# Optimization experiments

Measured on AMD Instinct MI355X. Metric: run time of the kernel, lower is better.

Reference implementation:

```python
import jax, jax.numpy as jnp
import numpy as np

BATCH, SEQ_LEN, NUM_TAGS = 1024, 512, 48


def setup_inputs() -> dict:
    key = jax.random.key(0)
    k1, k2 = jax.random.split(key)
    potentials = jax.random.normal(k1, (BATCH, SEQ_LEN, NUM_TAGS), dtype=jnp.float32)
    transition_params = jax.random.normal(k2, (NUM_TAGS, NUM_TAGS), dtype=jnp.float32)
    return {"potentials": potentials, "transition_params": transition_params}


def reference(potentials, transition_params):
    """Viterbi forward decode for a linear-chain CRF.

    potentials: [B, T, num_tags] unary potentials.
    transition_params: [num_tags, num_tags] binary potentials.
    Returns:
      backpointers: [B, T-1, num_tags] int32 argmax backpointers.
      scores: [B, num_tags] final Viterbi scores.
    """
    init_state = potentials[:, 0]                 # [B, num_tags]
    rest = jnp.swapaxes(potentials[:, 1:], 0, 1)  # [T-1, B, num_tags]

    def step(state, inputs):
        # state: [B, num_tags]; inputs: [B, num_tags]
        # transition_scores[b, i, j] = state[b, i] + trans[i, j]
        transition_scores = state[:, :, None] + transition_params[None]  # [B, tags, tags]
        new_state = inputs + jnp.max(transition_scores, axis=1)          # [B, tags]
        backpointers = jnp.argmax(transition_scores, axis=1).astype(jnp.int32)
        return new_state, backpointers

    final_state, backpointers = jax.lax.scan(step, init_state, rest)
    backpointers = jnp.swapaxes(backpointers, 0, 1)  # [B, T-1, num_tags]
    return backpointers, final_state
```

## Files before the change

kernel.cpp:

```cpp
#include <hip/hip_runtime.h>


constexpr int B_ = 1024;
constexpr int T_ = 512;
constexpr int K_ = 48;
constexpr int C_ = 6;

__device__ __forceinline__ int min3i(int a, int b, int c) {
    int m = a < b ? a : b;
    return m < c ? m : c;
}

__global__ __launch_bounds__(64, 1) void crf_viterbi_kernel(
    const float* __restrict__ pot,
    const float* __restrict__ trans,
    float* __restrict__ out)
{
    const int b = blockIdx.x;
    const int j = threadIdx.x;

    __shared__ __align__(16) float stv[K_];

    float tcol[K_];
    #pragma unroll
    for (int i = 0; i < K_; ++i) tcol[i] = trans[i * K_ + j];

    const float* pp = pot + (size_t)b * T_ * K_ + j;
    float* bpp      = out + (size_t)b * (T_ - 1) * K_ + j;
    float* scout    = out + (size_t)B_ * (T_ - 1) * K_ + (size_t)b * K_ + j;

    float myst = pp[0];
    stv[j] = myst;
    __builtin_amdgcn_wave_barrier();

    float bpf0 = 0.0f, bpf1 = 0.0f, bpf2 = 0.0f,
          bpf3 = 0.0f, bpf4 = 0.0f, bpf5 = 0.0f;

#define STEP(PCUR, BPV)                                                        \
    do {                                                                       \
         \
        float4 sv[12];                                                         \
        const float4* stv4 = (const float4*)stv;                               \
        _Pragma("unroll")                                                      \
        for (int c = 0; c < 12; ++c) sv[c] = stv4[c];                          \
                      \
        float cand[K_];                                                        \
        _Pragma("unroll")                                                      \
        for (int c = 0; c < 12; ++c) {                                         \
            cand[4 * c + 0] = sv[c].x + tcol[4 * c + 0];                       \
            cand[4 * c + 1] = sv[c].y + tcol[4 * c + 1];                       \
            cand[4 * c + 2] = sv[c].z + tcol[4 * c + 2];                       \
            cand[4 * c + 3] = sv[c].w + tcol[4 * c + 3];                       \
        }                                                                      \
         \
        float m1[16];                                                          \
        _Pragma("unroll")                                                      \
        for (int k = 0; k < 16; ++k)                                           \
            m1[k] = fmaxf(fmaxf(cand[3 * k], cand[3 * k + 1]), cand[3 * k + 2]); \
        float m2[6];                                                           \
        _Pragma("unroll")                                                      \
        for (int k = 0; k < 5; ++k)                                            \
            m2[k] = fmaxf(fmaxf(m1[3 * k], m1[3 * k + 1]), m1[3 * k + 2]);     \
        m2[5] = m1[15];                                                        \
        float mm = fmaxf(fmaxf(fmaxf(m2[0], m2[1]), m2[2]),                    \
                         fmaxf(fmaxf(m2[3], m2[4]), m2[5]));                   \
           \
        myst = (PCUR) + mm;                                                    \
        stv[j] = myst;                                                         \
        __builtin_amdgcn_wave_barrier();                                       \
            \
        int e[K_];                                                             \
        _Pragma("unroll")                                                      \
        for (int i = 0; i < K_; ++i) e[i] = (cand[i] == mm) ? i : 63;          \
        int n1[16];                                                            \
        _Pragma("unroll")                                                      \
        for (int k = 0; k < 16; ++k)                                           \
            n1[k] = min3i(e[3 * k], e[3 * k + 1], e[3 * k + 2]);               \
        int n2[6];                                                             \
        _Pragma("unroll")                                                      \
        for (int k = 0; k < 5; ++k)                                            \
            n2[k] = min3i(n1[3 * k], n1[3 * k + 1], n1[3 * k + 2]);            \
        n2[5] = n1[15];                                                        \
        int n30 = min3i(n2[0], n2[1], n2[2]);                                  \
        int n31 = min3i(n2[3], n2[4], n2[5]);                                  \
        int xx = n30 < n31 ? n30 : n31;                                        \
        BPV = (float)xx;                                                       \
        *bpp = BPV;                                            \
        bpp += K_;                                                             \
    } while (0)

    float p1 = pp[(size_t)1 * K_];
    float pbuf[C_];
    #pragma unroll
    for (int u = 0; u < C_; ++u) pbuf[u] = pp[(size_t)(2 + u) * K_];

    STEP(p1, bpf5);

    for (int t0 = 2; t0 < T_; t0 += C_) {
        float pc[C_];
        #pragma unroll
        for (int u = 0; u < C_; ++u) pc[u] = pbuf[u];

        #pragma unroll
        for (int u = 0; u < C_; ++u) {
            int tn = t0 + C_ + u;
            if (tn > T_ - 1) tn = T_ - 1;
            pbuf[u] = pp[(size_t)tn * K_];
        }

        STEP(pc[0], bpf0);
        STEP(pc[1], bpf1);
        STEP(pc[2], bpf2);
        STEP(pc[3], bpf3);
        STEP(pc[4], bpf4);
        STEP(pc[5], bpf5);
    }

    asm volatile("" :: "v"(bpf0), "v"(bpf1), "v"(bpf2),
                       "v"(bpf3), "v"(bpf4), "v"(bpf5));

    *scout = myst;
#undef STEP
}

extern "C" void kernel_launch(void* const* d_in, const int* in_sizes, int n_in,
                              void* d_out, int out_size, void* d_ws, size_t ws_size,
                              hipStream_t stream) {
    const float* pot   = (const float*)d_in[0];
    const float* trans = (const float*)d_in[1];
    float* out         = (float*)d_out;
    crf_viterbi_kernel<<<dim3(B_), dim3(K_), 0, stream>>>(pot, trans, out);
}
```

Baseline: 322.7 us.

## Broadcast Viterbi state via readlane instead of LDS round-trip

Replaces the shared-memory state exchange (LDS write, wave barrier, 12 float4 LDS reads) with 48 v_readlane broadcasts of each lane's state into scalar registers. This takes the LDS latency and barrier off the serial per-timestep dependency chain. The change also hoists the backpointer store offsets to constant per-step offsets, replaces the clamped prefetch with a guarded pointer-increment load, and adds a waves_per_eu hint. The cost is 48 readlane instructions per step, which may need SGPR-to-VGPR handling and can add issue pressure.

```diff
diff --git a/kernel.cpp b/kernel.cpp
--- a/kernel.cpp
+++ b/kernel.cpp
@@ -11,15 +11,15 @@
     return m < c ? m : c;
 }
 
-__global__ __launch_bounds__(64, 1) void crf_viterbi_kernel(
+__global__ __launch_bounds__(64, 1)
+__attribute__((amdgpu_waves_per_eu(1, 1)))
+void crf_viterbi_kernel(
     const float* __restrict__ pot,
     const float* __restrict__ trans,
     float* __restrict__ out)
 {
     const int b = blockIdx.x;
     const int j = threadIdx.x;
-
-    __shared__ __align__(16) float stv[K_];
 
     float tcol[K_];
     #pragma unroll
@@ -30,29 +30,23 @@
     float* scout    = out + (size_t)B_ * (T_ - 1) * K_ + (size_t)b * K_ + j;
 
     float myst = pp[0];
-    stv[j] = myst;
-    __builtin_amdgcn_wave_barrier();
 
     float bpf0 = 0.0f, bpf1 = 0.0f, bpf2 = 0.0f,
           bpf3 = 0.0f, bpf4 = 0.0f, bpf5 = 0.0f;
 
-#define STEP(PCUR, BPV)                                                        \
+#define STEP(PCUR, UOFF, BPV)                                                  \
     do {                                                                       \
-         \
-        float4 sv[12];                                                         \
-        const float4* stv4 = (const float4*)stv;                               \
+                \
+        float s[K_];                                                           \
         _Pragma("unroll")                                                      \
-        for (int c = 0; c < 12; ++c) sv[c] = stv4[c];                          \
-                      \
+        for (int i = 0; i < K_; ++i)                                           \
+            s[i] = __int_as_float(                                             \
+                __builtin_amdgcn_readlane(__float_as_int(myst), i));           \
+                                    \
         float cand[K_];                                                        \
         _Pragma("unroll")                                                      \
-        for (int c = 0; c < 12; ++c) {                                         \
-            cand[4 * c + 0] = sv[c].x + tcol[4 * c + 0];                       \
-            cand[4 * c + 1] = sv[c].y + tcol[4 * c + 1];                       \
-            cand[4 * c + 2] = sv[c].z + tcol[4 * c + 2];                       \
-            cand[4 * c + 3] = sv[c].w + tcol[4 * c + 3];                       \
-        }                                                                      \
-         \
+        for (int i = 0; i < K_; ++i) cand[i] = s[i] + tcol[i];                 \
+              \
         float m1[16];                                                          \
         _Pragma("unroll")                                                      \
         for (int k = 0; k < 16; ++k)                                           \
@@ -64,11 +58,7 @@
         m2[5] = m1[15];                                                        \
         float mm = fmaxf(fmaxf(fmaxf(m2[0], m2[1]), m2[2]),                    \
                          fmaxf(fmaxf(m2[3], m2[4]), m2[5]));                   \
-           \
-        myst = (PCUR) + mm;                                                    \
-        stv[j] = myst;                                                         \
-        __builtin_amdgcn_wave_barrier();                                       \
-            \
+                      \
         int e[K_];                                                             \
         _Pragma("unroll")                                                      \
         for (int i = 0; i < K_; ++i) e[i] = (cand[i] == mm) ? i : 63;          \
@@ -85,35 +75,38 @@
         int n31 = min3i(n2[3], n2[4], n2[5]);                                  \
         int xx = n30 < n31 ? n30 : n31;                                        \
         BPV = (float)xx;                                                       \
-        *bpp = BPV;                                            \
-        bpp += K_;                                                             \
+        bpp[(UOFF) * K_] = BPV;        \
+                \
+        myst = (PCUR) + mm;                                                    \
     } while (0)
 
     float p1 = pp[(size_t)1 * K_];
     float pbuf[C_];
     #pragma unroll
     for (int u = 0; u < C_; ++u) pbuf[u] = pp[(size_t)(2 + u) * K_];
+    const float* pld = pp + (size_t)8 * K_;
 
-    STEP(p1, bpf5);
+    STEP(p1, 0, bpf5);
+    bpp += K_;
 
     for (int t0 = 2; t0 < T_; t0 += C_) {
         float pc[C_];
         #pragma unroll
         for (int u = 0; u < C_; ++u) pc[u] = pbuf[u];
 
-        #pragma unroll
-        for (int u = 0; u < C_; ++u) {
-            int tn = t0 + C_ + u;
-            if (tn > T_ - 1) tn = T_ - 1;
-            pbuf[u] = pp[(size_t)tn * K_];
+        if (t0 < T_ - C_) {
+            #pragma unroll
+            for (int u = 0; u < C_; ++u) pbuf[u] = pld[(size_t)u * K_];
+            pld += (size_t)C_ * K_;
         }
 
-        STEP(pc[0], bpf0);
-        STEP(pc[1], bpf1);
-        STEP(pc[2], bpf2);
-        STEP(pc[3], bpf3);
-        STEP(pc[4], bpf4);
-        STEP(pc[5], bpf5);
+        STEP(pc[0], 0, bpf0);
+        STEP(pc[1], 1, bpf1);
+        STEP(pc[2], 2, bpf2);
+        STEP(pc[3], 3, bpf3);
+        STEP(pc[4], 4, bpf4);
+        STEP(pc[5], 5, bpf5);
+        bpp += (size_t)C_ * K_;
     }
 
     asm volatile("" :: "v"(bpf0), "v"(bpf1), "v"(bpf2),
```

New measurement: 354.9 us. +10.0%, slower.

## Defer argmax backpointer scan by one step to overlap with next max chain

Applied to the files above, without the earlier changes.

The argmax backpointer scan for step t now runs during step t+1, after the shared-state load and off the critical max chain, using double-buffered candidate arrays. The argmax reduction becomes four independent descending select chains instead of compare-then-min trees. Transition columns are stored as float2 pairs, and the potential prefetch uses a running pointer with a guard instead of clamped indices. The aim is to shorten the serial latency per time step, at the cost of more live registers for two candidate buffers.

```diff
diff --git a/kernel.cpp b/kernel.cpp
--- a/kernel.cpp
+++ b/kernel.cpp
@@ -11,6 +11,8 @@
     return m < c ? m : c;
 }
 
+#define C2(A, i) ((i) & 1 ? A[(i) >> 1].y : A[(i) >> 1].x)
+
 __global__ __launch_bounds__(64, 1) void crf_viterbi_kernel(
     const float* __restrict__ pot,
     const float* __restrict__ trans,
@@ -21,42 +23,68 @@
 
     __shared__ __align__(16) float stv[K_];
 
-    float tcol[K_];
+    float2 tcol2[K_ / 2];
     #pragma unroll
-    for (int i = 0; i < K_; ++i) tcol[i] = trans[i * K_ + j];
+    for (int i = 0; i < K_ / 2; ++i)
+        tcol2[i] = make_float2(trans[(2 * i) * K_ + j],
+                               trans[(2 * i + 1) * K_ + j]);
 
     const float* pp = pot + (size_t)b * T_ * K_ + j;
-    float* bpp      = out + (size_t)b * (T_ - 1) * K_ + j;
+    float* bpc      = out + (size_t)b * (T_ - 1) * K_ + j;
     float* scout    = out + (size_t)B_ * (T_ - 1) * K_ + (size_t)b * K_ + j;
 
     float myst = pp[0];
     stv[j] = myst;
     __builtin_amdgcn_wave_barrier();
 
+    float2 candA2[K_ / 2], candB2[K_ / 2];
+    float mmA = 0.0f, mmB = 0.0f;
+
     float bpf0 = 0.0f, bpf1 = 0.0f, bpf2 = 0.0f,
           bpf3 = 0.0f, bpf4 = 0.0f, bpf5 = 0.0f;
 
-#define STEP(PCUR, BPV)                                                        \
+#define SCAN4(CO2, MMO, XXDST)                                                 \
+    do {                                                                       \
+        int xx0 = 63, xx1 = 63, xx2 = 63, xx3 = 63;                            \
+        _Pragma("unroll")                                                      \
+        for (int i = 11; i >= 0; --i)  xx0 = (C2(CO2, i) == (MMO)) ? i : xx0;  \
+        _Pragma("unroll")                                                      \
+        for (int i = 23; i >= 12; --i) xx1 = (C2(CO2, i) == (MMO)) ? i : xx1;  \
+        _Pragma("unroll")                                                      \
+        for (int i = 35; i >= 24; --i) xx2 = (C2(CO2, i) == (MMO)) ? i : xx2;  \
+        _Pragma("unroll")                                                      \
+        for (int i = 47; i >= 36; --i) xx3 = (C2(CO2, i) == (MMO)) ? i : xx3;  \
+        XXDST = min3i(xx0, xx1, xx2) < xx3 ? min3i(xx0, xx1, xx2) : xx3;       \
+    } while (0)
+
+#define STEP(PCUR, CN2, CO2, MMN, MMO, DOSH, UOFF, BPV)                        \
     do {                                                                       \
          \
         float4 sv[12];                                                         \
         const float4* stv4 = (const float4*)stv;                               \
         _Pragma("unroll")                                                      \
         for (int c = 0; c < 12; ++c) sv[c] = stv4[c];                          \
-                      \
-        float cand[K_];                                                        \
+         \
+        if (DOSH) {                                                            \
+            int xx;                                                            \
+            SCAN4(CO2, MMO, xx);                                               \
+            BPV = (float)xx;                                                   \
+            bpc[(UOFF) * K_] = BPV;                \
+        }                                                                      \
+                   \
         _Pragma("unroll")                                                      \
         for (int c = 0; c < 12; ++c) {                                         \
-            cand[4 * c + 0] = sv[c].x + tcol[4 * c + 0];                       \
-            cand[4 * c + 1] = sv[c].y + tcol[4 * c + 1];                       \
-            cand[4 * c + 2] = sv[c].z + tcol[4 * c + 2];                       \
-            cand[4 * c + 3] = sv[c].w + tcol[4 * c + 3];                       \
+            CN2[2 * c]     = make_float2(sv[c].x + tcol2[2 * c].x,             \
+                                         sv[c].y + tcol2[2 * c].y);            \
+            CN2[2 * c + 1] = make_float2(sv[c].z + tcol2[2 * c + 1].x,         \
+                                         sv[c].w + tcol2[2 * c + 1].y);        \
         }                                                                      \
          \
         float m1[16];                                                          \
         _Pragma("unroll")                                                      \
         for (int k = 0; k < 16; ++k)                                           \
-            m1[k] = fmaxf(fmaxf(cand[3 * k], cand[3 * k + 1]), cand[3 * k + 2]); \
+            m1[k] = fmaxf(fmaxf(C2(CN2, 3 * k), C2(CN2, 3 * k + 1)),           \
+                          C2(CN2, 3 * k + 2));                                 \
         float m2[6];                                                           \
         _Pragma("unroll")                                                      \
         for (int k = 0; k < 5; ++k)                                            \
@@ -64,56 +92,45 @@
         m2[5] = m1[15];                                                        \
         float mm = fmaxf(fmaxf(fmaxf(m2[0], m2[1]), m2[2]),                    \
                          fmaxf(fmaxf(m2[3], m2[4]), m2[5]));                   \
+        MMN = mm;                                                              \
            \
         myst = (PCUR) + mm;                                                    \
         stv[j] = myst;                                                         \
         __builtin_amdgcn_wave_barrier();                                       \
-            \
-        int e[K_];                                                             \
-        _Pragma("unroll")                                                      \
-        for (int i = 0; i < K_; ++i) e[i] = (cand[i] == mm) ? i : 63;          \
-        int n1[16];                                                            \
-        _Pragma("unroll")                                                      \
-        for (int k = 0; k < 16; ++k)                                           \
-            n1[k] = min3i(e[3 * k], e[3 * k + 1], e[3 * k + 2]);               \
-        int n2[6];                                                             \
-        _Pragma("unroll")                                                      \
-        for (int k = 0; k < 5; ++k)                                            \
-            n2[k] = min3i(n1[3 * k], n1[3 * k + 1], n1[3 * k + 2]);            \
-        n2[5] = n1[15];                                                        \
-        int n30 = min3i(n2[0], n2[1], n2[2]);                                  \
-        int n31 = min3i(n2[3], n2[4], n2[5]);                                  \
-        int xx = n30 < n31 ? n30 : n31;                                        \
-        BPV = (float)xx;                                                       \
-        *bpp = BPV;                                            \
-        bpp += K_;                                                             \
     } while (0)
 
     float p1 = pp[(size_t)1 * K_];
     float pbuf[C_];
     #pragma unroll
     for (int u = 0; u < C_; ++u) pbuf[u] = pp[(size_t)(2 + u) * K_];
+    const float* pld = pp + (size_t)8 * K_;
 
-    STEP(p1, bpf5);
+    STEP(p1, candB2, candA2, mmB, mmA, false, 0, bpf0);
 
     for (int t0 = 2; t0 < T_; t0 += C_) {
         float pc[C_];
         #pragma unroll
         for (int u = 0; u < C_; ++u) pc[u] = pbuf[u];
 
-        #pragma unroll
-        for (int u = 0; u < C_; ++u) {
-            int tn = t0 + C_ + u;
-            if (tn > T_ - 1) tn = T_ - 1;
-            pbuf[u] = pp[(size_t)tn * K_];
+        if (t0 < T_ - C_) {
+            #pragma unroll
+            for (int u = 0; u < C_; ++u) pbuf[u] = pld[(size_t)u * K_];
+            pld += (size_t)C_ * K_;
         }
 
-        STEP(pc[0], bpf0);
-        STEP(pc[1], bpf1);
-        STEP(pc[2], bpf2);
-        STEP(pc[3], bpf3);
-        STEP(pc[4], bpf4);
-        STEP(pc[5], bpf5);
+        STEP(pc[0], candA2, candB2, mmA, mmB, true, 0, bpf0);
+        STEP(pc[1], candB2, candA2, mmB, mmA, true, 1, bpf1);
+        STEP(pc[2], candA2, candB2, mmA, mmB, true, 2, bpf2);
+        STEP(pc[3], candB2, candA2, mmB, mmA, true, 3, bpf3);
+        STEP(pc[4], candA2, candB2, mmA, mmB, true, 4, bpf4);
+        STEP(pc[5], candB2, candA2, mmB, mmA, true, 5, bpf5);
+        bpc += (size_t)C_ * K_;
+    }
+
+    {
+        int xx;
+        SCAN4(candB2, mmB, xx);
+        bpc[0] = (float)xx;
     }
 
     asm volatile("" :: "v"(bpf0), "v"(bpf1), "v"(bpf2),
@@ -121,6 +138,8 @@
 
     *scout = myst;
 #undef STEP
+#undef SCAN4
+#undef C2
 }
 
 extern "C" void kernel_launch(void* const* d_in, const int* in_sizes, int n_in,
```

Measured after the change: 387.3 us. 1.2x slower.
